# Kernel optimization log

Measured on AMD Instinct MI355X. Metric: run time of the kernel, lower is better.

The kernel has to match this reference:

```python
import jax, jax.numpy as jnp
import numpy as np

B, N, QD = 2, 4096, 1024
CD = 1024
H, DH = 8, 64
INNER = H * DH  # 512


def setup_inputs() -> dict:
    key = jax.random.key(0)
    ks = jax.random.split(key, 10)
    s = lambda d: (1.0 / np.sqrt(d)).astype(np.float32)
    return {
        "x": jax.random.normal(ks[0], (B, N, QD), dtype=jnp.float32),
        "context": jax.random.normal(ks[1], (B, N, CD), dtype=jnp.float32),
        "mask": jax.random.randint(ks[2], (B, N + 1), 0, 2) > 0,
        # weights stored as [in, out] (y = x @ W), matching torch Linear math
        "Wq": jax.random.normal(ks[3], (QD, INNER), dtype=jnp.float32) * s(QD),
        "Wk": jax.random.normal(ks[4], (CD, INNER), dtype=jnp.float32) * s(CD),
        "Wv": jax.random.normal(ks[5], (CD, INNER), dtype=jnp.float32) * s(CD),
        "Wk_bg": jax.random.normal(ks[6], (QD, INNER), dtype=jnp.float32) * s(QD),
        "Wv_bg": jax.random.normal(ks[7], (QD, INNER), dtype=jnp.float32) * s(QD),
        "Wout": jax.random.normal(ks[8], (INNER, QD), dtype=jnp.float32) * s(INNER),
        "b_out": jax.random.normal(ks[9], (QD,), dtype=jnp.float32) * 0.01,
    }


def reference(x, context, mask, Wq, Wk, Wv, Wk_bg, Wv_bg, Wout, b_out):
    b, n, _ = x.shape
    scale = DH ** -0.5

    q = x @ Wq                                             # [b, n, inner]
    pooled_x = jax.lax.stop_gradient(jnp.mean(x, axis=1, keepdims=True))  # [b, 1, qd]
    k = jnp.concatenate([context @ Wk, pooled_x @ Wk_bg], axis=1)  # [b, n+1, inner]
    v = jnp.concatenate([context @ Wv, pooled_x @ Wv_bg], axis=1)  # [b, n+1, inner]

    split = lambda t: t.reshape(b, t.shape[1], H, DH).transpose(0, 2, 1, 3)  # b h j d
    qh, kh, vh = split(q), split(k), split(v)

    sim = jnp.einsum('bhid,bhjd->bhij', qh, kh) * scale     # [b, h, n, n+1]
    neg = -jnp.finfo(sim.dtype).max
    sim = jnp.where(mask[:, None, None, :], sim, neg)
    attn = jax.nn.softmax(sim, axis=-1)
    out = jnp.einsum('bhij,bhjd->bhid', attn, vh)           # [b, h, n, d]
    out = out.transpose(0, 2, 1, 3).reshape(b, n, INNER)    # [b, n, inner]
    return out @ Wout + b_out                                # dropout p=0 -> identity
```

## Files before the change

### kernel.cpp

```cpp
#include <hip/hip_runtime.h>
#include <stdint.h>

#define N_TOK 4096
#define QDIM  1024
#define CDIM  1024
#define NH    8
#define DH    64
#define INNER 512
#define BATCH 2
#define N1    4097
#define N1P   4128
#define NJB   129
#define NJBP  130
#define VROWS 80
#define KTILE_SH 2048
#define VTILE_SH 2560

typedef __attribute__((ext_vector_type(8))) short short8;
typedef __attribute__((ext_vector_type(4))) float f32x4;
typedef __attribute__((ext_vector_type(4))) uint32_t u32x4;

__device__ __forceinline__ short f2bf(float f) {
    union { float f; uint32_t u; } x; x.f = f;
    uint32_t r = x.u + 0x7fffu + ((x.u >> 16) & 1u);
    return (short)(r >> 16);
}

__device__ __forceinline__ void async_copy16(void* lds, const void* g) {
    __builtin_amdgcn_global_load_lds(
        (const __attribute__((address_space(1))) void*)g,
        (__attribute__((address_space(3))) void*)lds, 16, 0, 0);
}

__global__ __launch_bounds__(256) void cast2_bf16_kernel(
        const float* __restrict__ a, const float* __restrict__ b,
        short* __restrict__ da, short* __restrict__ db, int n4) {
    int i = blockIdx.x * 256 + threadIdx.x;
    bool first = i < n4;
    const float* s = first ? a : b;
    short* d = first ? da : db;
    int j = first ? i : i - n4;
    float4 v = ((const float4*)s)[j];
    ((short4*)d)[j] = make_short4(f2bf(v.x), f2bf(v.y), f2bf(v.z), f2bf(v.w));
}

__global__ __launch_bounds__(256) void transpose_cast4_kernel(
        const float* __restrict__ Wq, const float* __restrict__ Wk,
        const float* __restrict__ Wv, const float* __restrict__ Wout,
        short* __restrict__ Wqt, short* __restrict__ Wkvt, short* __restrict__ Wot,
        float scale_q) {
    __shared__ float tile[32][33];
    int z = blockIdx.y;
    const float* W; short* Wt; int K, N; float scale = 1.f;
    if (z == 0)      { W = Wq;   Wt = Wqt;  K = QDIM;  N = INNER; scale = scale_q; }
    else if (z == 1) { W = Wk;   Wt = Wkvt; K = CDIM;  N = INNER; }
    else if (z == 2) { W = Wv;   Wt = Wkvt + (size_t)INNER * CDIM; K = CDIM; N = INNER; }
    else             { W = Wout; Wt = Wot;  K = INNER; N = QDIM; }
    int ntn = N >> 5;
    int bid = blockIdx.x;
    int n0 = (bid & (ntn - 1)) * 32, k0 = (bid / ntn) * 32;
    int tx = threadIdx.x & 31, ty = threadIdx.x >> 5;
    for (int r = ty; r < 32; r += 8)
        tile[r][tx] = W[(size_t)(k0 + r) * N + n0 + tx];
    __syncthreads();
    for (int r = ty; r < 32; r += 8)
        Wt[(size_t)(n0 + r) * K + k0 + tx] = f2bf(tile[tx][r] * scale);
}

__global__ __launch_bounds__(256) void pool_partial_kernel(
        const float* __restrict__ x, float* __restrict__ part) {
    int b = blockIdx.y, c = blockIdx.x;
    int t = threadIdx.x;
    float s0 = 0.f, s1 = 0.f, s2 = 0.f, s3 = 0.f;
    const float* xp = x + ((size_t)b * N_TOK + c * 128) * QDIM;
    for (int n = 0; n < 128; n++) {
        const float* row = xp + (size_t)n * QDIM;
        s0 += row[t];
        s1 += row[256 + t];
        s2 += row[512 + t];
        s3 += row[768 + t];
    }
    float* pp = part + ((size_t)b * 32 + c) * QDIM;
    pp[t] = s0; pp[256 + t] = s1; pp[512 + t] = s2; pp[768 + t] = s3;
}

__global__ __launch_bounds__(256) void bg_kernel(
        const float* __restrict__ part, const float* __restrict__ Wkbg,
        const float* __restrict__ Wvbg, short* __restrict__ kb, short* __restrict__ vb) {
    int b = blockIdx.x, jb = blockIdx.y, t = threadIdx.x;
    __shared__ float pooled[QDIM];
    for (int d = t; d < QDIM; d += 256) {
        float s = 0.f;
        for (int c = 0; c < 32; c++) s += part[((size_t)b * 32 + c) * QDIM + d];
        pooled[d] = s * (1.f / (float)N_TOK);
    }
    __syncthreads();
    int flat = jb * 256 + t;
    int matv = flat >> 9;
    int o = flat & 511;
    const float* W = matv ? Wvbg : Wkbg;
    float s = 0.f;
    for (int k = 0; k < QDIM; k++) s += pooled[k] * W[(size_t)k * INNER + o];
    int h = o >> 6, d = o & 63;
    if (matv) {
        vb[(((size_t)(b * NH + h)) * N1P + N_TOK) * DH + d] = f2bf(s);
    } else {
        kb[((size_t)(b * NH + h)) * NJBP * KTILE_SH + 128 * KTILE_SH
           + (d >> 5) * 1024 + (d & 31)] = f2bf(s);
    }
    if (jb == 0) {
        for (int idx = t; idx < NH * 31 * DH; idx += 256) {
            int h2 = idx / (31 * DH);
            int r2 = idx % (31 * DH);
            int rr = 1 + r2 / DH;
            int d2 = r2 % DH;
            kb[((size_t)(b * NH + h2)) * NJBP * KTILE_SH + 128 * KTILE_SH
               + (d2 >> 5) * 1024 + rr * 32 + (d2 & 31)] = 0;
        }
        for (int idx = t; idx < NH * KTILE_SH; idx += 256) {
            int h2 = idx >> 11;
            int off = idx & (KTILE_SH - 1);
            kb[((size_t)(b * NH + h2)) * NJBP * KTILE_SH + 129 * KTILE_SH + off] = 0;
        }
    }
}

__global__ __launch_bounds__(256) void transpose_v_kernel(
        const short* __restrict__ vin, short* __restrict__ vout,
        const int* __restrict__ mask) {
    __shared__ short tile[32][65];
    __shared__ int mloc[32];
    int bh = blockIdx.z, b = bh >> 3;
    int j0 = blockIdx.x * 32, jb = blockIdx.x;
    int tx = threadIdx.x & 63, ty = threadIdx.x >> 6;
    const short* src = vin + (size_t)bh * N1P * DH;
    if (j0 < N1P) {
        for (int r = ty; r < 32; r += 4)
            tile[r][tx] = src[(size_t)(j0 + r) * DH + tx];
    }
    if (threadIdx.x < 32) {
        int j = j0 + threadIdx.x;
        mloc[threadIdx.x] = (j < N1) ? mask[b * N1 + j] : 0;
    }
    __syncthreads();
    int tp = threadIdx.x & 31, dy = threadIdx.x >> 5;
    int s = (tp >> 3) * 4 + (tp & 3) + ((tp >> 2) & 1) * 16;
    bool mk = mloc[s] != 0;
    short* dst = vout + ((size_t)bh * NJBP + jb) * VTILE_SH;
    for (int d = dy; d < DH; d += 8) {
        int swz = (((tp >> 3) ^ ((d >> 1) & 3)) << 3) | (tp & 7);
        dst[d * 32 + swz] = mk ? tile[s][d] : (short)0;
    }
    if (dy == 0) dst[64 * 32 + tp] = mk ? (short)0x3F80 : (short)0;
    if (dy == 1)
        for (int d = 65; d < 80; d++) dst[d * 32 + tp] = 0;
}

__global__ __launch_bounds__(256) void qkv_gemm_kernel(
        const short* __restrict__ x_bf, const short* __restrict__ c_bf,
        const short* __restrict__ Wqt, const short* __restrict__ Wkvt,
        short* __restrict__ q_bf, short* __restrict__ k_bf, short* __restrict__ v_tmp) {
    __shared__ short As[128 * 32];
    __shared__ short Bs[128 * 32];
    const int t = threadIdx.x;
    const int lane = t & 63, w = t >> 6;
    const int wr = w >> 1, wc = w & 1;
    const int lo = lane & 15, g = lane >> 4;
    const int arow = lane >> 2;
    const int ac8 = (lane & 3) * 8;

    const short *A, *W;
    int m0, n0, which;
    int bid = (blockIdx.x & 7) * 96 + (blockIdx.x >> 3);
    if (bid < 256) { A = x_bf; W = Wqt;  m0 = (bid >> 2) * 128; n0 = (bid & 3) * 128; which = 0; }
    else { int i = bid - 256; A = c_bf; W = Wkvt; m0 = (i >> 3) * 128; n0 = (i & 7) * 128;
           which = (n0 < 512) ? 1 : 2; }

    f32x4 acc[4][4] = {};
    for (int k0 = 0; k0 < 1024; k0 += 32) {
        for (int q = 0; q < 2; q++) {
            int seg = w * 2 + q;
            async_copy16(&As[seg * 512], A + (size_t)(m0 + seg * 16 + arow) * 1024 + k0 + ac8);
            async_copy16(&Bs[seg * 512], W + (size_t)(n0 + seg * 16 + arow) * 1024 + k0 + ac8);
        }
        __syncthreads();
        short8 af[4], bfv[4];
        #pragma unroll
        for (int i = 0; i < 4; i++)
            af[i] = *(const short8*)&As[(wr * 64 + i * 16 + lo) * 32 + g * 8];
        #pragma unroll
        for (int j = 0; j < 4; j++)
            bfv[j] = *(const short8*)&Bs[(wc * 64 + j * 16 + lo) * 32 + g * 8];
        #pragma unroll
        for (int i = 0; i < 4; i++)
            #pragma unroll
            for (int j = 0; j < 4; j++)
                acc[i][j] = __builtin_amdgcn_mfma_f32_16x16x32_bf16(af[i], bfv[j], acc[i][j], 0, 0, 0);
        __syncthreads();
    }

    if (which == 0) {
        #pragma unroll
        for (int i = 0; i < 4; i++)
            #pragma unroll
            for (int j = 0; j < 4; j++) {
                int row = m0 + wr * 64 + i * 16 + g * 4;
                int col0 = n0 + wc * 64 + j * 16 + lo;
                int h = col0 >> 6, d = col0 & 63;
                f32x4 v = acc[i][j];
                #pragma unroll
                for (int r = 0; r < 4; r++) {
                    int m = row + r;
                    int b = m >> 12, ii = m & 4095;
                    q_bf[(((size_t)(b * NH + h)) * N_TOK + ii) * DH + d] = f2bf(v[r]);
                }
            }
    } else if (which == 1) {
        #pragma unroll
        for (int i = 0; i < 4; i++)
            #pragma unroll
            for (int j = 0; j < 4; j++) {
                int row = m0 + wr * 64 + i * 16 + g * 4;
                int col0 = n0 + wc * 64 + j * 16 + lo;
                int h = col0 >> 6, d = col0 & 63;
                f32x4 v = acc[i][j];
                #pragma unroll
                for (int r = 0; r < 4; r++) {
                    int m = row + r;
                    int b = m >> 12, ii = m & 4095;
                    int off = (d >> 5) * 1024 + (ii & 31) * 32 + (d & 31);
                    off ^= ((ii >> 1) & 3) << 3;
                    k_bf[((size_t)(b * NH + h)) * NJBP * KTILE_SH + (ii >> 5) * KTILE_SH
                         + off] = f2bf(v[r]);
                }
            }
    } else {
        #pragma unroll
        for (int i = 0; i < 4; i++)
            #pragma unroll
            for (int j = 0; j < 4; j++) {
                int row = m0 + wr * 64 + i * 16 + g * 4;
                int col0 = n0 + wc * 64 + j * 16 + lo;
                int col = col0 - 512;
                int h = col >> 6, d = col & 63;
                f32x4 v = acc[i][j];
                #pragma unroll
                for (int r = 0; r < 4; r++) {
                    int m = row + r;
                    int b = m >> 12, ii = m & 4095;
                    v_tmp[(((size_t)(b * NH + h)) * N1P + ii) * DH + d] = f2bf(v[r]);
                }
            }
    }
}

__global__ __launch_bounds__(256) void out_gemm_kernel(
        const short* __restrict__ A, const short* __restrict__ Wt,
        float* __restrict__ outf, const float* __restrict__ bias) {
    __shared__ short As[128 * 32];
    __shared__ short Bs[128 * 32];
    const int t = threadIdx.x;
    const int lane = t & 63, w = t >> 6;
    const int wr = w >> 1, wc = w & 1;
    const int lo = lane & 15, g = lane >> 4;
    const int arow = lane >> 2;
    const int ac8 = (lane & 3) * 8;
    const int m0 = blockIdx.x * 128, n0 = blockIdx.y * 128;

    f32x4 acc[4][4] = {};
    for (int k0 = 0; k0 < INNER; k0 += 32) {
        for (int q = 0; q < 2; q++) {
            int seg = w * 2 + q;
            async_copy16(&As[seg * 512], A + (size_t)(m0 + seg * 16 + arow) * INNER + k0 + ac8);
            async_copy16(&Bs[seg * 512], Wt + (size_t)(n0 + seg * 16 + arow) * INNER + k0 + ac8);
        }
        __syncthreads();
        short8 af[4], bfv[4];
        #pragma unroll
        for (int i = 0; i < 4; i++)
            af[i] = *(const short8*)&As[(wr * 64 + i * 16 + lo) * 32 + g * 8];
        #pragma unroll
        for (int j = 0; j < 4; j++)
            bfv[j] = *(const short8*)&Bs[(wc * 64 + j * 16 + lo) * 32 + g * 8];
        #pragma unroll
        for (int i = 0; i < 4; i++)
            #pragma unroll
            for (int j = 0; j < 4; j++)
                acc[i][j] = __builtin_amdgcn_mfma_f32_16x16x32_bf16(af[i], bfv[j], acc[i][j], 0, 0, 0);
        __syncthreads();
    }
    #pragma unroll
    for (int i = 0; i < 4; i++)
        #pragma unroll
        for (int j = 0; j < 4; j++) {
            int row = m0 + wr * 64 + i * 16 + g * 4;
            int col = n0 + wc * 64 + j * 16 + lo;
            f32x4 v = acc[i][j];
            #pragma unroll
            for (int r = 0; r < 4; r++)
                outf[(size_t)(row + r) * QDIM + col] = v[r] + bias[col];
        }
}

__global__ __launch_bounds__(256, 2) void attn_kernel(
        const short* __restrict__ qb,
        const short* __restrict__ kb,
        const short* __restrict__ vtb,
        short* __restrict__ ob) {
    const int t = threadIdx.x, lane = t & 63, w = t >> 6;
    const int lo = lane & 15, g = lane >> 4;
    const int gs = g ^ ((lo >> 1) & 3);
    const int id = blockIdx.x;
    const int h = id & 7, b = (id >> 3) & 1, qt = id >> 4;
    const int q0 = qt * 128 + w * 32;
    const size_t bh = (size_t)(b * NH + h);

    const short* qp = qb + (bh * N_TOK + q0 + lo) * DH;
    short8 qa[2][2];
    qa[0][0] = *(const short8*)(qp + g * 8);
    qa[0][1] = *(const short8*)(qp + 32 + g * 8);
    qa[1][0] = *(const short8*)(qp + 16 * DH + g * 8);
    qa[1][1] = *(const short8*)(qp + 16 * DH + 32 + g * 8);

    __shared__ short Kl[2][2][KTILE_SH];
    __shared__ short Vl[2][2][VTILE_SH];

    const short* ksrc = kb + bh * (size_t)NJBP * KTILE_SH + w * 512 + lane * 8;
    const short* vsrc = vtb + bh * (size_t)NJBP * VTILE_SH + w * 512 + lane * 8;

    f32x4 o[2][5] = {};
    f32x4 z = {};

    async_copy16(&Kl[0][0][w * 512], ksrc);
    async_copy16(&Vl[0][0][w * 512], vsrc);
    async_copy16(&Kl[0][1][w * 512], ksrc + KTILE_SH);
    async_copy16(&Vl[0][1][w * 512], vsrc + VTILE_SH);
    if (w == 0) {
        async_copy16(&Vl[0][0][2048], vsrc + 2048);
        async_copy16(&Vl[0][1][2048], vsrc + VTILE_SH + 2048);
    }
    __syncthreads();

    for (int it = 0; it < 65; ++it) {
        const int cur = it & 1;
        if (it < 64) {
            const short* ks = ksrc + (size_t)(2 * it + 2) * KTILE_SH;
            const short* vs = vsrc + (size_t)(2 * it + 2) * VTILE_SH;
            async_copy16(&Kl[cur ^ 1][0][w * 512], ks);
            async_copy16(&Vl[cur ^ 1][0][w * 512], vs);
            async_copy16(&Kl[cur ^ 1][1][w * 512], ks + KTILE_SH);
            async_copy16(&Vl[cur ^ 1][1][w * 512], vs + VTILE_SH);
            if (w == 0) {
                async_copy16(&Vl[cur ^ 1][0][2048], vs + 2048);
                async_copy16(&Vl[cur ^ 1][1][2048], vs + VTILE_SH + 2048);
            }
        }
        #pragma unroll
        for (int sub = 0; sub < 2; ++sub) {
            const short* kl = &Kl[cur][sub][0];
            const short* vl = &Vl[cur][sub][0];
            __builtin_amdgcn_s_setprio(1);
            short8 kf00 = *(const short8*)&kl[(lo) * 32 + gs * 8];
            short8 kf01 = *(const short8*)&kl[1024 + (lo) * 32 + gs * 8];
            short8 kf10 = *(const short8*)&kl[(16 + lo) * 32 + gs * 8];
            short8 kf11 = *(const short8*)&kl[1024 + (16 + lo) * 32 + gs * 8];
            short8 vfr[5];
            #pragma unroll
            for (int f = 0; f < 5; f++)
                vfr[f] = *(const short8*)&vl[(f * 16 + lo) * 32 + gs * 8];
            #pragma unroll
            for (int rg = 0; rg < 2; rg++) {
                f32x4 s0 = __builtin_amdgcn_mfma_f32_16x16x32_bf16(kf00, qa[rg][0], z, 0, 0, 0);
                s0 = __builtin_amdgcn_mfma_f32_16x16x32_bf16(kf01, qa[rg][1], s0, 0, 0, 0);
                f32x4 s1 = __builtin_amdgcn_mfma_f32_16x16x32_bf16(kf10, qa[rg][0], z, 0, 0, 0);
                s1 = __builtin_amdgcn_mfma_f32_16x16x32_bf16(kf11, qa[rg][1], s1, 0, 0, 0);
                uint32_t u0 = __float_as_uint(__builtin_amdgcn_exp2f(s0[0])) + 0x8000u;
                uint32_t u1 = __float_as_uint(__builtin_amdgcn_exp2f(s0[1])) + 0x8000u;
                uint32_t u2 = __float_as_uint(__builtin_amdgcn_exp2f(s0[2])) + 0x8000u;
                uint32_t u3 = __float_as_uint(__builtin_amdgcn_exp2f(s0[3])) + 0x8000u;
                uint32_t u4 = __float_as_uint(__builtin_amdgcn_exp2f(s1[0])) + 0x8000u;
                uint32_t u5 = __float_as_uint(__builtin_amdgcn_exp2f(s1[1])) + 0x8000u;
                uint32_t u6 = __float_as_uint(__builtin_amdgcn_exp2f(s1[2])) + 0x8000u;
                uint32_t u7 = __float_as_uint(__builtin_amdgcn_exp2f(s1[3])) + 0x8000u;
                u32x4 pr;
                pr[0] = __builtin_amdgcn_perm(u1, u0, 0x07060302u);
                pr[1] = __builtin_amdgcn_perm(u3, u2, 0x07060302u);
                pr[2] = __builtin_amdgcn_perm(u5, u4, 0x07060302u);
                pr[3] = __builtin_amdgcn_perm(u7, u6, 0x07060302u);
                short8 pa = __builtin_bit_cast(short8, pr);
                #pragma unroll
                for (int f = 0; f < 5; f++)
                    o[rg][f] = __builtin_amdgcn_mfma_f32_16x16x32_bf16(pa, vfr[f], o[rg][f], 0, 0, 0);
            }
            __builtin_amdgcn_s_setprio(0);
        }
        __syncthreads();
    }

    short* op = ob + ((size_t)(b * N_TOK) + q0) * INNER + h * DH;
    #pragma unroll
    for (int rg = 0; rg < 2; rg++)
        #pragma unroll
        for (int r = 0; r < 4; r++) {
            float l = __shfl(o[rg][4][r], lane & 48);
            float inv = (l > 0.f) ? 1.f / l : 0.f;
            short* o_ = op + (size_t)(rg * 16 + g * 4 + r) * INNER;
            o_[lo]      = f2bf(o[rg][0][r] * inv);
            o_[16 + lo] = f2bf(o[rg][1][r] * inv);
            o_[32 + lo] = f2bf(o[rg][2][r] * inv);
            o_[48 + lo] = f2bf(o[rg][3][r] * inv);
        }
}

extern "C" void kernel_launch(void* const* d_in, const int* in_sizes, int n_in,
                              void* d_out, int out_size, void* d_ws, size_t ws_size,
                              hipStream_t stream) {
    const float* x    = (const float*)d_in[0];
    const float* ctx  = (const float*)d_in[1];
    const int*   mask = (const int*)d_in[2];
    const float* Wq   = (const float*)d_in[3];
    const float* Wk   = (const float*)d_in[4];
    const float* Wv   = (const float*)d_in[5];
    const float* Wkbg = (const float*)d_in[6];
    const float* Wvbg = (const float*)d_in[7];
    const float* Wout = (const float*)d_in[8];
    const float* bout = (const float*)d_in[9];
    float* out = (float*)d_out;

    char* p = (char*)d_ws;
    auto alloc = [&](size_t b) { char* r = p; p += (b + 255) & ~(size_t)255; return r; };
    short* x_bf  = (short*)alloc((size_t)BATCH * N_TOK * QDIM * 2);
    short* c_bf  = (short*)alloc((size_t)BATCH * N_TOK * CDIM * 2);
    short* Wqt   = (short*)alloc((size_t)INNER * QDIM * 2);
    short* Wkvt  = (short*)alloc((size_t)2 * INNER * CDIM * 2);
    short* Wot   = (short*)alloc((size_t)QDIM * INNER * 2);
    short* q_bf  = (short*)alloc((size_t)BATCH * NH * N_TOK * DH * 2);
    short* k_bf  = (short*)alloc((size_t)BATCH * NH * NJBP * KTILE_SH * 2);
    short* v_tmp = (short*)alloc((size_t)BATCH * NH * N1P * DH * 2);
    short* vt_bf = (short*)alloc((size_t)BATCH * NH * NJBP * VTILE_SH * 2);
    short* o_bf  = (short*)alloc((size_t)BATCH * N_TOK * INNER * 2);
    float* part  = (float*)alloc((size_t)BATCH * 32 * QDIM * 4);

    const float SCALE_Q = 0.125f * 1.4426950408889634f;

    int n4 = BATCH * N_TOK * QDIM / 4;
    cast2_bf16_kernel<<<(2 * n4 + 255) / 256, 256, 0, stream>>>(x, ctx, x_bf, c_bf, n4);

    transpose_cast4_kernel<<<dim3(512, 4), 256, 0, stream>>>(
        Wq, Wk, Wv, Wout, Wqt, Wkvt, Wot, SCALE_Q);

    pool_partial_kernel<<<dim3(32, BATCH), 256, 0, stream>>>(x, part);

    qkv_gemm_kernel<<<768, 256, 0, stream>>>(x_bf, c_bf, Wqt, Wkvt, q_bf, k_bf, v_tmp);

    bg_kernel<<<dim3(BATCH, 4), 256, 0, stream>>>(part, Wkbg, Wvbg, k_bf, v_tmp);
    transpose_v_kernel<<<dim3(NJBP, 1, BATCH * NH), 256, 0, stream>>>(v_tmp, vt_bf, mask);

    attn_kernel<<<512, 256, 0, stream>>>(q_bf, k_bf, vt_bf, o_bf);

    out_gemm_kernel<<<dim3(64, 8), 256, 0, stream>>>(o_bf, Wot, out, bout);
}
```

Measured before the change: 319.3 us.

## Fuse prep kernels, fold bg projection into QKV GEMM, widen attention K/V staging

New measurement: 308.1 us. 1.04x faster.

```diff
diff --git a/kernel.cpp b/kernel.cpp
--- a/kernel.cpp
+++ b/kernel.cpp
@@ -11,7 +11,7 @@
 #define N1    4097
 #define N1P   4128
 #define NJB   129
-#define NJBP  130
+#define NJBP  132
 #define VROWS 80
 #define KTILE_SH 2048
 #define VTILE_SH 2560
@@ -32,96 +32,57 @@
         (__attribute__((address_space(3))) void*)lds, 16, 0, 0);
 }
 
-__global__ __launch_bounds__(256) void cast2_bf16_kernel(
-        const float* __restrict__ a, const float* __restrict__ b,
-        short* __restrict__ da, short* __restrict__ db, int n4) {
-    int i = blockIdx.x * 256 + threadIdx.x;
-    bool first = i < n4;
-    const float* s = first ? a : b;
-    short* d = first ? da : db;
-    int j = first ? i : i - n4;
-    float4 v = ((const float4*)s)[j];
-    ((short4*)d)[j] = make_short4(f2bf(v.x), f2bf(v.y), f2bf(v.z), f2bf(v.w));
-}
-
-__global__ __launch_bounds__(256) void transpose_cast4_kernel(
+#define NB_CAST 16384
+#define NB_TC   2048
+#define NB_POOL 64
+__global__ __launch_bounds__(256) void prep_kernel(
+        const float* __restrict__ x, const float* __restrict__ ctx,
         const float* __restrict__ Wq, const float* __restrict__ Wk,
         const float* __restrict__ Wv, const float* __restrict__ Wout,
+        short* __restrict__ x_bf, short* __restrict__ c_bf,
         short* __restrict__ Wqt, short* __restrict__ Wkvt, short* __restrict__ Wot,
-        float scale_q) {
+        float* __restrict__ part, float scale_q) {
     __shared__ float tile[32][33];
-    int z = blockIdx.y;
-    const float* W; short* Wt; int K, N; float scale = 1.f;
-    if (z == 0)      { W = Wq;   Wt = Wqt;  K = QDIM;  N = INNER; scale = scale_q; }
-    else if (z == 1) { W = Wk;   Wt = Wkvt; K = CDIM;  N = INNER; }
-    else if (z == 2) { W = Wv;   Wt = Wkvt + (size_t)INNER * CDIM; K = CDIM; N = INNER; }
-    else             { W = Wout; Wt = Wot;  K = INNER; N = QDIM; }
-    int ntn = N >> 5;
-    int bid = blockIdx.x;
-    int n0 = (bid & (ntn - 1)) * 32, k0 = (bid / ntn) * 32;
-    int tx = threadIdx.x & 31, ty = threadIdx.x >> 5;
-    for (int r = ty; r < 32; r += 8)
-        tile[r][tx] = W[(size_t)(k0 + r) * N + n0 + tx];
-    __syncthreads();
-    for (int r = ty; r < 32; r += 8)
-        Wt[(size_t)(n0 + r) * K + k0 + tx] = f2bf(tile[tx][r] * scale);
-}
-
-__global__ __launch_bounds__(256) void pool_partial_kernel(
-        const float* __restrict__ x, float* __restrict__ part) {
-    int b = blockIdx.y, c = blockIdx.x;
-    int t = threadIdx.x;
-    float s0 = 0.f, s1 = 0.f, s2 = 0.f, s3 = 0.f;
-    const float* xp = x + ((size_t)b * N_TOK + c * 128) * QDIM;
-    for (int n = 0; n < 128; n++) {
-        const float* row = xp + (size_t)n * QDIM;
-        s0 += row[t];
-        s1 += row[256 + t];
-        s2 += row[512 + t];
-        s3 += row[768 + t];
-    }
-    float* pp = part + ((size_t)b * 32 + c) * QDIM;
-    pp[t] = s0; pp[256 + t] = s1; pp[512 + t] = s2; pp[768 + t] = s3;
-}
-
-__global__ __launch_bounds__(256) void bg_kernel(
-        const float* __restrict__ part, const float* __restrict__ Wkbg,
-        const float* __restrict__ Wvbg, short* __restrict__ kb, short* __restrict__ vb) {
-    int b = blockIdx.x, jb = blockIdx.y, t = threadIdx.x;
-    __shared__ float pooled[QDIM];
-    for (int d = t; d < QDIM; d += 256) {
-        float s = 0.f;
-        for (int c = 0; c < 32; c++) s += part[((size_t)b * 32 + c) * QDIM + d];
-        pooled[d] = s * (1.f / (float)N_TOK);
-    }
-    __syncthreads();
-    int flat = jb * 256 + t;
-    int matv = flat >> 9;
-    int o = flat & 511;
-    const float* W = matv ? Wvbg : Wkbg;
-    float s = 0.f;
-    for (int k = 0; k < QDIM; k++) s += pooled[k] * W[(size_t)k * INNER + o];
-    int h = o >> 6, d = o & 63;
-    if (matv) {
-        vb[(((size_t)(b * NH + h)) * N1P + N_TOK) * DH + d] = f2bf(s);
+    int blk = blockIdx.x, t = threadIdx.x;
+    if (blk < NB_CAST) {
+        const int n4 = BATCH * N_TOK * QDIM / 4;
+        int i = blk * 256 + t;
+        bool first = i < n4;
+        const float* s = first ? x : ctx;
+        short* d = first ? x_bf : c_bf;
+        int j = first ? i : i - n4;
+        float4 v = ((const float4*)s)[j];
+        ((short4*)d)[j] = make_short4(f2bf(v.x), f2bf(v.y), f2bf(v.z), f2bf(v.w));
+    } else if (blk < NB_CAST + NB_TC) {
+        int rel = blk - NB_CAST;
+        int z = rel >> 9, bid = rel & 511;
+        const float* W; short* Wt; int K, N; float scale = 1.f;
+        if (z == 0)      { W = Wq;   Wt = Wqt;  K = QDIM;  N = INNER; scale = scale_q; }
+        else if (z == 1) { W = Wk;   Wt = Wkvt; K = CDIM;  N = INNER; }
+        else if (z == 2) { W = Wv;   Wt = Wkvt + (size_t)INNER * CDIM; K = CDIM; N = INNER; }
+        else             { W = Wout; Wt = Wot;  K = INNER; N = QDIM; }
+        int ntn = N >> 5;
+        int n0 = (bid & (ntn - 1)) * 32, k0 = (bid / ntn) * 32;
+        int tx = t & 31, ty = t >> 5;
+        for (int r = ty; r < 32; r += 8)
+            tile[r][tx] = W[(size_t)(k0 + r) * N + n0 + tx];
+        __syncthreads();
+        for (int r = ty; r < 32; r += 8)
+            Wt[(size_t)(n0 + r) * K + k0 + tx] = f2bf(tile[tx][r] * scale);
     } else {
-        kb[((size_t)(b * NH + h)) * NJBP * KTILE_SH + 128 * KTILE_SH
-           + (d >> 5) * 1024 + (d & 31)] = f2bf(s);
-    }
-    if (jb == 0) {
-        for (int idx = t; idx < NH * 31 * DH; idx += 256) {
-            int h2 = idx / (31 * DH);
-            int r2 = idx % (31 * DH);
-            int rr = 1 + r2 / DH;
-            int d2 = r2 % DH;
-            kb[((size_t)(b * NH + h2)) * NJBP * KTILE_SH + 128 * KTILE_SH
-               + (d2 >> 5) * 1024 + rr * 32 + (d2 & 31)] = 0;
-        }
-        for (int idx = t; idx < NH * KTILE_SH; idx += 256) {
-            int h2 = idx >> 11;
-            int off = idx & (KTILE_SH - 1);
-            kb[((size_t)(b * NH + h2)) * NJBP * KTILE_SH + 129 * KTILE_SH + off] = 0;
-        }
+        int rel = blk - NB_CAST - NB_TC;
+        int c = rel & 31, b = rel >> 5;
+        float s0 = 0.f, s1 = 0.f, s2 = 0.f, s3 = 0.f;
+        const float* xp = x + ((size_t)b * N_TOK + c * 128) * QDIM;
+        for (int n = 0; n < 128; n++) {
+            const float* row = xp + (size_t)n * QDIM;
+            s0 += row[t];
+            s1 += row[256 + t];
+            s2 += row[512 + t];
+            s3 += row[768 + t];
+        }
+        float* pp = part + ((size_t)b * 32 + c) * QDIM;
+        pp[t] = s0; pp[256 + t] = s1; pp[512 + t] = s2; pp[768 + t] = s3;
     }
 }
 
@@ -159,10 +120,55 @@
 __global__ __launch_bounds__(256) void qkv_gemm_kernel(
         const short* __restrict__ x_bf, const short* __restrict__ c_bf,
         const short* __restrict__ Wqt, const short* __restrict__ Wkvt,
+        const float* __restrict__ part, const float* __restrict__ Wkbg,
+        const float* __restrict__ Wvbg,
         short* __restrict__ q_bf, short* __restrict__ k_bf, short* __restrict__ v_tmp) {
     __shared__ short As[128 * 32];
     __shared__ short Bs[128 * 32];
+    __shared__ float pooled[QDIM];
     const int t = threadIdx.x;
+    int bid = (blockIdx.x & 7) * 97 + (blockIdx.x >> 3);
+
+    if (bid >= 768) {
+        int sub = bid - 768;
+        int b = sub & 1, jb = sub >> 1;
+        for (int d = t; d < QDIM; d += 256) {
+            float s = 0.f;
+            for (int c = 0; c < 32; c++) s += part[((size_t)b * 32 + c) * QDIM + d];
+            pooled[d] = s * (1.f / (float)N_TOK);
+        }
+        __syncthreads();
+        int flat = jb * 256 + t;
+        int matv = flat >> 9;
+        int o = flat & 511;
+        const float* W = matv ? Wvbg : Wkbg;
+        float s = 0.f;
+        for (int k = 0; k < QDIM; k++) s += pooled[k] * W[(size_t)k * INNER + o];
+        int h = o >> 6, d = o & 63;
+        if (matv) {
+            v_tmp[(((size_t)(b * NH + h)) * N1P + N_TOK) * DH + d] = f2bf(s);
+        } else {
+            k_bf[((size_t)(b * NH + h)) * NJBP * KTILE_SH + 128 * KTILE_SH
+                 + (d >> 5) * 1024 + (d & 31)] = f2bf(s);
+        }
+        if (jb == 0) {
+            for (int idx = t; idx < NH * 31 * DH; idx += 256) {
+                int h2 = idx / (31 * DH);
+                int r2 = idx % (31 * DH);
+                int rr = 1 + r2 / DH;
+                int d2 = r2 % DH;
+                k_bf[((size_t)(b * NH + h2)) * NJBP * KTILE_SH + 128 * KTILE_SH
+                     + (d2 >> 5) * 1024 + rr * 32 + (d2 & 31)] = 0;
+            }
+            for (int idx = t; idx < NH * 3 * KTILE_SH; idx += 256) {
+                int h2 = idx / (3 * KTILE_SH);
+                int r2 = idx % (3 * KTILE_SH);
+                k_bf[((size_t)(b * NH + h2)) * NJBP * KTILE_SH + 129 * KTILE_SH + r2] = 0;
+            }
+        }
+        return;
+    }
+
     const int lane = t & 63, w = t >> 6;
     const int wr = w >> 1, wc = w & 1;
     const int lo = lane & 15, g = lane >> 4;
@@ -171,7 +177,6 @@
 
     const short *A, *W;
     int m0, n0, which;
-    int bid = (blockIdx.x & 7) * 96 + (blockIdx.x >> 3);
     if (bid < 256) { A = x_bf; W = Wqt;  m0 = (bid >> 2) * 128; n0 = (bid & 3) * 128; which = 0; }
     else { int i = bid - 256; A = c_bf; W = Wkvt; m0 = (i >> 3) * 128; n0 = (i & 7) * 128;
            which = (n0 < 512) ? 1 : 2; }
@@ -265,7 +270,8 @@
     const int lo = lane & 15, g = lane >> 4;
     const int arow = lane >> 2;
     const int ac8 = (lane & 3) * 8;
-    const int m0 = blockIdx.x * 128, n0 = blockIdx.y * 128;
+    const int bid = (blockIdx.x & 7) * 64 + (blockIdx.x >> 3);
+    const int m0 = (bid & 63) * 128, n0 = (bid >> 6) * 128;
 
     f32x4 acc[4][4] = {};
     for (int k0 = 0; k0 < INNER; k0 += 32) {
@@ -322,8 +328,8 @@
     qa[1][0] = *(const short8*)(qp + 16 * DH + g * 8);
     qa[1][1] = *(const short8*)(qp + 16 * DH + 32 + g * 8);
 
-    __shared__ short Kl[2][2][KTILE_SH];
-    __shared__ short Vl[2][2][VTILE_SH];
+    __shared__ short Kl[2][4][KTILE_SH];
+    __shared__ short Vl[2][4][VTILE_SH];
 
     const short* ksrc = kb + bh * (size_t)NJBP * KTILE_SH + w * 512 + lane * 8;
     const short* vsrc = vtb + bh * (size_t)NJBP * VTILE_SH + w * 512 + lane * 8;
@@ -331,32 +337,28 @@
     f32x4 o[2][5] = {};
     f32x4 z = {};
 
-    async_copy16(&Kl[0][0][w * 512], ksrc);
-    async_copy16(&Vl[0][0][w * 512], vsrc);
-    async_copy16(&Kl[0][1][w * 512], ksrc + KTILE_SH);
-    async_copy16(&Vl[0][1][w * 512], vsrc + VTILE_SH);
-    if (w == 0) {
-        async_copy16(&Vl[0][0][2048], vsrc + 2048);
-        async_copy16(&Vl[0][1][2048], vsrc + VTILE_SH + 2048);
+    #pragma unroll
+    for (int s = 0; s < 4; s++) {
+        async_copy16(&Kl[0][s][w * 512], ksrc + (size_t)s * KTILE_SH);
+        async_copy16(&Vl[0][s][w * 512], vsrc + (size_t)s * VTILE_SH);
+        if (w == 0) async_copy16(&Vl[0][s][2048], vsrc + (size_t)s * VTILE_SH + 2048);
     }
     __syncthreads();
 
-    for (int it = 0; it < 65; ++it) {
+    for (int it = 0; it < 33; ++it) {
         const int cur = it & 1;
-        if (it < 64) {
-            const short* ks = ksrc + (size_t)(2 * it + 2) * KTILE_SH;
-            const short* vs = vsrc + (size_t)(2 * it + 2) * VTILE_SH;
-            async_copy16(&Kl[cur ^ 1][0][w * 512], ks);
-            async_copy16(&Vl[cur ^ 1][0][w * 512], vs);
-            async_copy16(&Kl[cur ^ 1][1][w * 512], ks + KTILE_SH);
-            async_copy16(&Vl[cur ^ 1][1][w * 512], vs + VTILE_SH);
-            if (w == 0) {
-                async_copy16(&Vl[cur ^ 1][0][2048], vs + 2048);
-                async_copy16(&Vl[cur ^ 1][1][2048], vs + VTILE_SH + 2048);
-            }
-        }
-        #pragma unroll
-        for (int sub = 0; sub < 2; ++sub) {
+        if (it < 32) {
+            const short* ks = ksrc + (size_t)(4 * it + 4) * KTILE_SH;
+            const short* vs = vsrc + (size_t)(4 * it + 4) * VTILE_SH;
+            #pragma unroll
+            for (int s = 0; s < 4; s++) {
+                async_copy16(&Kl[cur ^ 1][s][w * 512], ks + (size_t)s * KTILE_SH);
+                async_copy16(&Vl[cur ^ 1][s][w * 512], vs + (size_t)s * VTILE_SH);
+                if (w == 0) async_copy16(&Vl[cur ^ 1][s][2048], vs + (size_t)s * VTILE_SH + 2048);
+            }
+        }
+        #pragma unroll
+        for (int sub = 0; sub < 4; ++sub) {
             const short* kl = &Kl[cur][sub][0];
             const short* vl = &Vl[cur][sub][0];
             __builtin_amdgcn_s_setprio(1);
@@ -443,20 +445,15 @@
 
     const float SCALE_Q = 0.125f * 1.4426950408889634f;
 
-    int n4 = BATCH * N_TOK * QDIM / 4;
-    cast2_bf16_kernel<<<(2 * n4 + 255) / 256, 256, 0, stream>>>(x, ctx, x_bf, c_bf, n4);
-
-    transpose_cast4_kernel<<<dim3(512, 4), 256, 0, stream>>>(
-        Wq, Wk, Wv, Wout, Wqt, Wkvt, Wot, SCALE_Q);
-
-    pool_partial_kernel<<<dim3(32, BATCH), 256, 0, stream>>>(x, part);
-
-    qkv_gemm_kernel<<<768, 256, 0, stream>>>(x_bf, c_bf, Wqt, Wkvt, q_bf, k_bf, v_tmp);
-
-    bg_kernel<<<dim3(BATCH, 4), 256, 0, stream>>>(part, Wkbg, Wvbg, k_bf, v_tmp);
+    prep_kernel<<<NB_CAST + NB_TC + NB_POOL, 256, 0, stream>>>(
+        x, ctx, Wq, Wk, Wv, Wout, x_bf, c_bf, Wqt, Wkvt, Wot, part, SCALE_Q);
+
+    qkv_gemm_kernel<<<776, 256, 0, stream>>>(
+        x_bf, c_bf, Wqt, Wkvt, part, Wkbg, Wvbg, q_bf, k_bf, v_tmp);
+
     transpose_v_kernel<<<dim3(NJBP, 1, BATCH * NH), 256, 0, stream>>>(v_tmp, vt_bf, mask);
 
     attn_kernel<<<512, 256, 0, stream>>>(q_bf, k_bf, vt_bf, o_bf);
 
-    out_gemm_kernel<<<dim3(64, 8), 256, 0, stream>>>(o_bf, Wot, out, bout);
-}
+    out_gemm_kernel<<<512, 256, 0, stream>>>(o_bf, Wot, out, bout);
+}
```
